# Kernel optimization log

Hardware: AMD Instinct MI355X
Metric: run time of the kernel (lower is better)

The kernel has to match this reference:

```python
import jax, jax.numpy as jnp
import numpy as np

N = 2048      # agent_num
H = 2048      # hid_size
OBS = 1024    # obs_size
A = 64        # action_dim
ITERS = 3     # comm_iters
B = 1         # batch (structurally 1: original does gate.view(1,n,n))
STD = 0.02


def setup_inputs() -> dict:
    key = jax.random.key(0)
    ks = jax.random.split(key, 10)
    f = lambda k, shp: (jax.random.normal(k, shp, jnp.float32) * STD)
    return {
        "obs": jax.random.normal(ks[0], (B, N, OBS), jnp.float32),
        "alive_mask": jnp.ones((N,), jnp.float32),
        "enc_w": f(ks[1], (H, OBS)),
        "enc_b": jnp.zeros((H,), jnp.float32),
        "g_w": f(ks[2], (N, H)),
        "g_b": jnp.zeros((N,), jnp.float32),
        "w_ih": f(ks[3], (4 * H, H)),
        "w_hh": f(ks[4], (4 * H, H)),
        "b_ih": f(ks[5], (4 * H,)),
        "b_hh": f(ks[6], (4 * H,)),
        "act_w": f(ks[7], (A, H)),
        "act_b": jnp.zeros((A,), jnp.float32),
        "val_w": f(ks[8], (1, H)),
        "val_b": jnp.zeros((1,), jnp.float32),
    }


def reference(obs, alive_mask, enc_w, enc_b, g_w, g_b, w_ih, w_hh,
              b_ih, b_hh, act_w, act_b, val_w, val_b):
    b, n, _ = obs.shape
    hid = enc_w.shape[0]
    # state encoder: tanh(Linear(obs))
    e = jnp.tanh(jnp.einsum('bno,ho->bnh', obs, enc_w) + enc_b)  # (B,n,H)
    h = jnp.zeros((b, n, hid), obs.dtype)
    cell = jnp.zeros((b, n, hid), obs.dtype)
    comm_mask = 1.0 - jnp.eye(n, dtype=obs.dtype)                # (n,n), no self-comm
    n_alive = jnp.sum(alive_mask)
    alive_pair = alive_mask[:, None] * alive_mask[None, :]       # alive[j]*alive[i]
    static_w = comm_mask * alive_pair / (n_alive - 1.0)          # (n,n)

    for it in range(ITERS):
        # hard gate: ceil(sigmoid(g(h)))  -> (B, n_sender, n_receiver)
        gate = jnp.ceil(jax.nn.sigmoid(jnp.einsum('bjh,kh->bjk', h, g_w) + g_b))
        G = gate * static_w                                      # (B,n,n)
        # masked gated broadcast-sum over sender agents j (fused, no (B,n,n,H))
        if it == 0:
            c = jnp.zeros_like(h)
        else:
            c = jnp.einsum('bji,bjh->bih', G, h)
        inp = e + c                                              # (B,n,H)
        # torch.nn.LSTMCell, gate order (i, f, g, o)
        z = (jnp.einsum('bnh,gh->bng', inp, w_ih)
             + jnp.einsum('bnh,gh->bng', h, w_hh) + b_ih + b_hh)
        zi, zf, zg, zo = jnp.split(z, 4, axis=-1)
        cell = jax.nn.sigmoid(zf) * cell + jax.nn.sigmoid(zi) * jnp.tanh(zg)
        h = jax.nn.sigmoid(zo) * jnp.tanh(cell)

    log_p = jax.nn.log_softmax(jnp.einsum('bnh,ah->bna', h, act_w) + act_b, axis=-1)
    value = jnp.einsum('bnh,vh->bnv', h, val_w) + val_b
    return log_p, value
```

## Files before the change

### kernel.cpp

```cpp
#include <hip/hip_runtime.h>
#include <cmath>

#define N_AG 2048
#define HID  2048
#define OBSD 1024
#define ACT  64
#define GATES (4*HID)

typedef short s16x8 __attribute__((ext_vector_type(8)));
typedef short s16x4 __attribute__((ext_vector_type(4)));
typedef float f32x4 __attribute__((ext_vector_type(4)));

__device__ __forceinline__ unsigned short f2bf(float f) {
  union { float f; unsigned u; } v; v.f = f;
  return (unsigned short)((v.u + 0x7FFFu + ((v.u >> 16) & 1u)) >> 16);
}
__device__ __forceinline__ float bf2f(unsigned short u) {
  union { float f; unsigned u; } v; v.u = ((unsigned)u) << 16;
  return v.f;
}
__device__ __forceinline__ float sigm(float x) { return 1.0f / (1.0f + expf(-x)); }

__device__ __forceinline__ void gload16(const unsigned short* g, unsigned short* l) {
  __builtin_amdgcn_global_load_lds(
      (const __attribute__((address_space(1))) void*)g,
      (__attribute__((address_space(3))) void*)l, 16, 0, 0);
}


template <int MODE>
__global__ __launch_bounds__(512, 2) void gemm256(
    const unsigned short* __restrict__ A, const unsigned short* __restrict__ B,
    int K, int lda, int ldb,
    unsigned short* __restrict__ E1b, const float* __restrict__ q,
    const float* __restrict__ bc, float* __restrict__ cell,
    unsigned short* __restrict__ hN)
{
  __shared__ __align__(16) unsigned short As[32768];
  __shared__ __align__(16) unsigned short Bs[32768];

  const int tid  = threadIdx.x;
  const int lane = tid & 63;
  const int wave = tid >> 6;
  const int wm   = wave >> 2, wn = wave & 3;
  const int quad = lane >> 4, l16 = lane & 15, r7 = lane & 7;
  const long tileM = (long)blockIdx.y * 256;
  const long tileN = (long)blockIdx.x * 256;

  const unsigned scol  = (((lane & 7) ^ (lane >> 3)) * 8u);
  const unsigned aoffL = (unsigned)(tileM + wave * 8 + (lane >> 3)) * (unsigned)lda + scol;
  const unsigned boffL = (unsigned)(tileN + (wave >> 2) * 64 + (wave & 3) * 8 + (lane >> 3))
                           * (unsigned)ldb + scol;

#define ST_A(d, h, t) { \
    gload16(A + aoffL + (unsigned)((h) * 64) * (unsigned)lda + (unsigned)(t) * 64u, \
            &As[(d) * 16384 + (h) * 8192 + wave * 512]); \
    gload16(A + aoffL + (unsigned)(128 + (h) * 64) * (unsigned)lda + (unsigned)(t) * 64u, \
            &As[(d) * 16384 + (h) * 8192 + wave * 512 + 4096]); }
#define ST_B(d, h, t) { \
    gload16(B + boffL + (unsigned)((h) * 32) * (unsigned)ldb + (unsigned)(t) * 64u, \
            &Bs[(d) * 16384 + (h) * 8192 + wave * 512]); \
    gload16(B + boffL + (unsigned)(128 + (h) * 32) * (unsigned)ldb + (unsigned)(t) * 64u, \
            &Bs[(d) * 16384 + (h) * 8192 + wave * 512 + 4096]); }

  const int ax = wm * 4096 + l16 * 64;
  const int bx = wn * 2048 + l16 * 64;
  const int c0 = (quad ^ r7) * 8;
  const int c1 = ((4 + quad) ^ r7) * 8;

  s16x8 af0[4][2], af1[4][2], bA[2][2], bB[2][2];
  f32x4 acc[8][4] = {};

#define LD_A(d, Mh, dst) { const unsigned short* p_ = &As[(d) * 16384 + (Mh) * 8192 + ax]; \
    _Pragma("unroll") for (int ml = 0; ml < 4; ++ml) { \
      dst[ml][0] = *(const s16x8*)(p_ + ml * 1024 + c0); \
      dst[ml][1] = *(const s16x8*)(p_ + ml * 1024 + c1); } }
#define LD_B(d, Nh, dst) { const unsigned short* p_ = &Bs[(d) * 16384 + (Nh) * 8192 + bx]; \
    _Pragma("unroll") for (int nl = 0; nl < 2; ++nl) { \
      dst[nl][0] = *(const s16x8*)(p_ + nl * 1024 + c0); \
      dst[nl][1] = *(const s16x8*)(p_ + nl * 1024 + c1); } }
#define QMM(Mh, Nh, afv, bb) \
    _Pragma("unroll") for (int ks = 0; ks < 2; ++ks) \
    _Pragma("unroll") for (int ml = 0; ml < 4; ++ml) \
    _Pragma("unroll") for (int nl = 0; nl < 2; ++nl) \
      acc[(Mh) * 4 + ml][(Nh) * 2 + nl] = __builtin_amdgcn_mfma_f32_16x16x32_bf16( \
          afv[ml][ks], bb[nl][ks], acc[(Mh) * 4 + ml][(Nh) * 2 + nl], 0, 0, 0);
#define BAR  __builtin_amdgcn_s_barrier()
#define SCHB __builtin_amdgcn_sched_barrier(0)

  const int NT = K >> 6;

  ST_B(0, 0, 0); ST_A(0, 0, 0); ST_B(0, 1, 0); ST_A(0, 1, 0);
  asm volatile("s_waitcnt vmcnt(0)" ::: "memory");
  BAR;
  LD_A(0, 0, af0); LD_B(0, 0, bA);

  for (int t = 0; t < NT; ++t) {
    const int cur = t & 1, nxt = cur ^ 1;
    const bool s1 = (t + 1 < NT);
    LD_B(cur, 1, bB);
    if (s1) { ST_B(nxt, 0, t + 1); ST_A(nxt, 0, t + 1); }
    SCHB;
    __builtin_amdgcn_s_setprio(1); QMM(0, 0, af0, bA); __builtin_amdgcn_s_setprio(0);
    if (s1) { asm volatile("s_waitcnt vmcnt(4)" ::: "memory"); }
    else    { asm volatile("s_waitcnt vmcnt(0)" ::: "memory"); }
    BAR;
    LD_A(cur, 1, af1);
    if (s1) ST_B(nxt, 1, t + 1);
    SCHB;
    __builtin_amdgcn_s_setprio(1); QMM(0, 1, af0, bB); __builtin_amdgcn_s_setprio(0);
    if (s1) { asm volatile("s_waitcnt vmcnt(2)" ::: "memory"); }
    BAR;
    if (s1) ST_A(nxt, 1, t + 1);
    SCHB;
    __builtin_amdgcn_s_setprio(1); QMM(1, 0, af1, bA); __builtin_amdgcn_s_setprio(0);
    if (s1) LD_B(nxt, 0, bA);
    BAR;
    if (s1) LD_A(nxt, 0, af0);
    SCHB;
    __builtin_amdgcn_s_setprio(1); QMM(1, 1, af1, bB); __builtin_amdgcn_s_setprio(0);
    if (s1) { asm volatile("s_waitcnt vmcnt(2)" ::: "memory"); }
    BAR;
  }

  const int cb0 = (int)tileN + wn * 64;
  const int hid = ((cb0 >> 6) << 4) | l16;
  float bcv[4], qv[4];
#pragma unroll
  for (int g = 0; g < 4; ++g) {
    bcv[g] = bc[cb0 + g * 16 + l16];
    qv[g]  = (MODE == 11) ? q[cb0 + g * 16 + l16] : 0.f;
  }
#pragma unroll
  for (int mf = 0; mf < 8; ++mf) {
    long ag0 = tileM + wm * 128 + mf * 16 + quad * 4;
#pragma unroll
    for (int r = 0; r < 4; ++r) {
      long ag = ag0 + r;
      size_t eb_i = (size_t)ag * GATES + cb0 + l16;
      float zi = acc[mf][0][r], zf = acc[mf][1][r];
      float zg = acc[mf][2][r], zo = acc[mf][3][r];
      if (MODE == 10) {
        E1b[eb_i]      = f2bf(zi);
        E1b[eb_i + 16] = f2bf(zf);
        E1b[eb_i + 32] = f2bf(zg);
        E1b[eb_i + 48] = f2bf(zo);
        zi += bcv[0]; zf += bcv[1]; zg += bcv[2]; zo += bcv[3];
      } else {
        zi += bf2f(E1b[eb_i])      + qv[0] + bcv[0];
        zf += bf2f(E1b[eb_i + 16]) + qv[1] + bcv[1];
        zg += bf2f(E1b[eb_i + 32]) + qv[2] + bcv[2];
        zo += bf2f(E1b[eb_i + 48]) + qv[3] + bcv[3];
      }
      float cold = (MODE == 10) ? 0.f : cell[(size_t)ag * HID + hid];
      float cnew = sigm(zf) * cold + sigm(zi) * tanhf(zg);
      float hv   = sigm(zo) * tanhf(cnew);
      cell[(size_t)ag * HID + hid] = cnew;
      hN[(size_t)ag * HID + hid]   = f2bf(hv);
    }
  }
#undef ST_A
#undef ST_B
#undef LD_A
#undef LD_B
#undef QMM
#undef BAR
#undef SCHB
}

template <int MODE>
__global__ __launch_bounds__(256, 4) void gemm_bt(
    const unsigned short* __restrict__ A, const unsigned short* __restrict__ B,
    int K, int lda, int ldb,
    unsigned short* __restrict__ Cb, float* __restrict__ Cf, int ldc,
    const float* __restrict__ bias)
{
  __shared__ __align__(16) unsigned short As0[2 * 128 * 32];
  __shared__ __align__(16) unsigned short Bs0[2 * 128 * 32];
  const int tid  = threadIdx.x;
  const int lane = tid & 63;
  const int wave = tid >> 6;
  const int wm = wave >> 1, wn = wave & 1;
  const int quad = lane >> 4, l16 = lane & 15;
  const long tileM = (long)blockIdx.y * 128;
  const long tileN = (long)blockIdx.x * 128;
  const long koff  = (long)blockIdx.z * K;

  const int srow = lane >> 2;
  const int skc  = (lane & 3) * 8;
  const unsigned short* gA = &A[(tileM + wave * 32 + srow) * lda + koff + skc];
  const unsigned short* gB = &B[(tileN + wave * 32 + srow) * ldb + koff + skc];
  const int ldsOff = wave * 32 * 32;

  f32x4 acc[4][4] = {};
  const int nIt = K >> 5;

  gload16(gA, &As0[ldsOff]);
  gload16(gA + 16 * lda, &As0[ldsOff + 16 * 32]);
  gload16(gB, &Bs0[ldsOff]);
  gload16(gB + 16 * ldb, &Bs0[ldsOff + 16 * 32]);

  for (int i = 0; i < nIt; ++i) {
    __syncthreads();
    const int cb = (i & 1) * 4096;
    if (i + 1 < nIt) {
      const int nb = ((i + 1) & 1) * 4096;
      const long ko = (long)(i + 1) * 32;
      gload16(gA + ko, &As0[nb + ldsOff]);
      gload16(gA + ko + 16 * lda, &As0[nb + ldsOff + 16 * 32]);
      gload16(gB + ko, &Bs0[nb + ldsOff]);
      gload16(gB + ko + 16 * ldb, &Bs0[nb + ldsOff + 16 * 32]);
    }
    s16x8 af[4], bfr[4];
#pragma unroll
    for (int ii = 0; ii < 4; ++ii)
      af[ii] = *(const s16x8*)&As0[cb + (wm * 64 + ii * 16 + l16) * 32 + quad * 8];
#pragma unroll
    for (int j = 0; j < 4; ++j)
      bfr[j] = *(const s16x8*)&Bs0[cb + (wn * 64 + j * 16 + l16) * 32 + quad * 8];
#pragma unroll
    for (int ii = 0; ii < 4; ++ii)
#pragma unroll
      for (int j = 0; j < 4; ++j)
        acc[ii][j] = __builtin_amdgcn_mfma_f32_16x16x32_bf16(af[ii], bfr[j], acc[ii][j], 0, 0, 0);
  }

#pragma unroll
  for (int i = 0; i < 4; ++i) {
    long r0 = tileM + wm * 64 + i * 16 + quad * 4;
#pragma unroll
    for (int j = 0; j < 4; ++j) {
      long col = tileN + wn * 64 + j * 16 + l16;
      float bv = (MODE == 1) ? bias[col] : 0.f;
#pragma unroll
      for (int r = 0; r < 4; ++r) {
        float v = acc[i][j][r];
        if (MODE == 1) { v = tanhf(v + bv); Cb[(r0 + r) * ldc + col] = f2bf(v); }
        if (MODE == 2) atomicAdd(&Cf[(r0 + r) * ldc + col], v);
      }
    }
  }
}

__global__ void cvt4_dual(const float* __restrict__ inA, unsigned short* __restrict__ outA,
                          const float* __restrict__ inB, unsigned short* __restrict__ outB) {
  int i = blockIdx.x * 256 + threadIdx.x;
  f32x4 a = ((const f32x4*)inA)[i];
  f32x4 b = ((const f32x4*)inB)[i];
  s16x4 oa, ob;
#pragma unroll
  for (int c = 0; c < 4; ++c) { oa[c] = (short)f2bf(a[c]); ob[c] = (short)f2bf(b[c]); }
  ((s16x4*)outA)[i] = oa;
  ((s16x4*)outB)[i] = ob;
}

__global__ void buildw(const float* __restrict__ w_ih, const float* __restrict__ w_hh,
                       const float* __restrict__ nA,
                       unsigned short* __restrict__ Wihb, unsigned short* __restrict__ W2b) {
  int i = blockIdx.x * 256 + threadIdx.x;
  float s = 1.0f / (nA[0] - 1.0f);
  int c  = i >> 9;
  int kk = (i & 511) * 4;
  int g   = (c >> 4) & 3;
  int hid = ((c >> 6) << 4) | (c & 15);
  size_t src = ((size_t)g * HID + hid) * HID + kk;
  size_t dst = (size_t)c * HID + kk;
  f32x4 a = *(const f32x4*)&w_ih[src];
  f32x4 b = *(const f32x4*)&w_hh[src];
  s16x4 oa, ob;
#pragma unroll
  for (int e = 0; e < 4; ++e) {
    oa[e] = (short)f2bf(a[e]);
    ob[e] = (short)f2bf(b[e] - s * a[e]);
  }
  *(s16x4*)&Wihb[dst] = oa;
  *(s16x4*)&W2b[dst] = ob;
}

__global__ void build_whd(const float* __restrict__ act_w, const float* __restrict__ val_w,
                          unsigned short* __restrict__ whd) {
  int i = blockIdx.x * 256 + threadIdx.x;
  int r = i >> 9;
  int k = (i & 511) * 4;
  f32x4 v = {0.f, 0.f, 0.f, 0.f};
  if (r < 64)       v = *(const f32x4*)&act_w[(size_t)r * HID + k];
  else if (r == 64) v = *(const f32x4*)&val_w[k];
  s16x4 o;
  o[0] = (short)f2bf(v[0]); o[1] = (short)f2bf(v[1]);
  o[2] = (short)f2bf(v[2]); o[3] = (short)f2bf(v[3]);
  *(s16x4*)&whd[(size_t)r * HID + k] = o;
}

__global__ void biasmix(const float* __restrict__ b_ih, const float* __restrict__ b_hh,
                        float* __restrict__ bc) {
  int i = blockIdx.x * 256 + threadIdx.x;
  if (i < GATES) {
    int g   = (i >> 4) & 3;
    int hid = ((i >> 6) << 4) | (i & 15);
    int src = g * HID + hid;
    bc[i] = b_ih[src] + b_hh[src];
  }
}

__global__ void nalive_k(const float* __restrict__ alive, float* __restrict__ nA) {
  __shared__ float red[256];
  float s = 0.f;
  for (int i = threadIdx.x; i < N_AG; i += 256) s += alive[i];
  red[threadIdx.x] = s;
  __syncthreads();
  for (int st = 128; st > 0; st >>= 1) {
    if (threadIdx.x < st) red[threadIdx.x] += red[threadIdx.x + st];
    __syncthreads();
  }
  if (threadIdx.x == 0) nA[0] = red[0];
}

__global__ void colsum(const unsigned short* __restrict__ hb, const float* __restrict__ alive,
                       float* __restrict__ S) {
  int hid = blockIdx.x * 256 + threadIdx.x;
  int r0 = blockIdx.y * 128;
  float s = 0.f;
  for (int n = r0; n < r0 + 128; ++n) s += alive[n] * bf2f(hb[(size_t)n * HID + hid]);
  atomicAdd(&S[hid], s);
}

__global__ __launch_bounds__(256) void gemv_q(const unsigned short* __restrict__ Wihb,
                                              const float* __restrict__ S,
                                              const float* __restrict__ nA,
                                              float* __restrict__ q) {
  __shared__ float Sl[HID];
  int tid = threadIdx.x, lane = tid & 63, wave = tid >> 6;
  for (int k = tid; k < HID; k += 256) Sl[k] = S[k];
  __syncthreads();
  int g = blockIdx.x * 4 + wave;
  const unsigned short* wr = Wihb + (size_t)g * HID;
  float acc = 0.f;
#pragma unroll
  for (int c = 0; c < 4; ++c) {
    int k = c * 512 + lane * 8;
    s16x8 w = *(const s16x8*)&wr[k];
#pragma unroll
    for (int e = 0; e < 8; ++e) acc += bf2f((unsigned short)w[e]) * Sl[k + e];
  }
  for (int off = 32; off; off >>= 1) acc += __shfl_xor(acc, off);
  if (lane == 0) q[g] = acc / (nA[0] - 1.0f);
}

__global__ __launch_bounds__(256) void head_ep(const float* __restrict__ zh,
                                               const float* __restrict__ act_b,
                                               const float* __restrict__ val_b,
                                               float* __restrict__ out) {
  int wave = threadIdx.x >> 6, lane = threadIdx.x & 63;
  int row = blockIdx.x * 4 + wave;
  const float* zr = zh + (size_t)row * 128;
  float a = zr[lane] + act_b[lane];
  float m = a;
  for (int off = 32; off; off >>= 1) m = fmaxf(m, __shfl_xor(m, off));
  float ex = expf(a - m), s = ex;
  for (int off = 32; off; off >>= 1) s += __shfl_xor(s, off);
  out[(size_t)row * ACT + lane] = a - m - logf(s);
  if (lane == 0) out[(size_t)N_AG * ACT + row] = zr[64] + val_b[0];
}

extern "C" void kernel_launch(void* const* d_in, const int* in_sizes, int n_in,
                              void* d_out, int out_size, void* d_ws, size_t ws_size,
                              hipStream_t stream) {
  const float* obs   = (const float*)d_in[0];
  const float* alive = (const float*)d_in[1];
  const float* enc_w = (const float*)d_in[2];
  const float* enc_b = (const float*)d_in[3];
  const float* w_ih  = (const float*)d_in[6];
  const float* w_hh  = (const float*)d_in[7];
  const float* b_ih  = (const float*)d_in[8];
  const float* b_hh  = (const float*)d_in[9];
  const float* act_w = (const float*)d_in[10];
  const float* act_b = (const float*)d_in[11];
  const float* val_w = (const float*)d_in[12];
  const float* val_b = (const float*)d_in[13];
  float* out = (float*)d_out;

  char* p = (char*)d_ws;
  unsigned short* Wihb = (unsigned short*)p; p += (size_t)GATES * HID * 2;
  unsigned short* W2b  = (unsigned short*)p; p += (size_t)GATES * HID * 2;
  unsigned short* E1b  = (unsigned short*)p; p += (size_t)N_AG * GATES * 2;
  unsigned short* obsb = (unsigned short*)p; p += (size_t)N_AG * OBSD * 2;
  unsigned short* encb = (unsigned short*)p; p += (size_t)HID * OBSD * 2;
  unsigned short* eb   = (unsigned short*)p; p += (size_t)N_AG * HID * 2;
  unsigned short* h0   = (unsigned short*)p; p += (size_t)N_AG * HID * 2;
  unsigned short* h1   = (unsigned short*)p; p += (size_t)N_AG * HID * 2;
  unsigned short* Whd  = (unsigned short*)p; p += (size_t)128 * HID * 2;
  float* cell = (float*)p; p += (size_t)N_AG * HID * 4;
  float* zh   = (float*)p; p += (size_t)N_AG * 128 * 4;
  float* bc   = (float*)p; p += GATES * 4;
  float* q    = (float*)p; p += GATES * 4;
  float* S    = (float*)p; p += HID * 4;
  float* nA   = (float*)p; p += 256;

  cvt4_dual<<<(N_AG * OBSD / 4) / 256, 256, 0, stream>>>(obs, obsb, enc_w, encb);
  nalive_k<<<1, 256, 0, stream>>>(alive, nA);
  buildw<<<((size_t)GATES * HID / 4) / 256, 256, 0, stream>>>(w_ih, w_hh, nA, Wihb, W2b);
  build_whd<<<(128 * HID / 4) / 256, 256, 0, stream>>>(act_w, val_w, Whd);
  biasmix<<<GATES / 256, 256, 0, stream>>>(b_ih, b_hh, bc);

  gemm_bt<1><<<dim3(HID / 128, N_AG / 128), 256, 0, stream>>>(
      obsb, encb, OBSD, OBSD, OBSD, eb, nullptr, HID, enc_b);

  gemm256<10><<<dim3(GATES / 256, N_AG / 256), 512, 0, stream>>>(
      eb, Wihb, HID, HID, HID, E1b, nullptr, bc, cell, h0);

  unsigned short* hcur = h0;
  unsigned short* hnxt = h1;
  for (int it = 1; it < 3; ++it) {
    hipMemsetAsync(S, 0, HID * 4, stream);
    colsum<<<dim3(HID / 256, 16), 256, 0, stream>>>(hcur, alive, S);
    gemv_q<<<GATES / 4, 256, 0, stream>>>(Wihb, S, nA, q);
    gemm256<11><<<dim3(GATES / 256, N_AG / 256), 512, 0, stream>>>(
        hcur, W2b, HID, HID, HID, E1b, q, bc, cell, hnxt);
    unsigned short* tmp = hcur; hcur = hnxt; hnxt = tmp;
  }

  hipMemsetAsync(zh, 0, (size_t)N_AG * 128 * 4, stream);
  gemm_bt<2><<<dim3(1, N_AG / 128, 8), 256, 0, stream>>>(
      hcur, Whd, HID / 8, HID, HID, nullptr, zh, 128, nullptr);
  head_ep<<<N_AG / 4, 256, 0, stream>>>(zh, act_b, val_b, out);
}
```

Baseline: 537.2 us.

## Fuse alive-weighted column sum into LSTM GEMM epilogue and pack per-thread state

The separate colsum kernel is removed. Each LSTM GEMM epilogue now accumulates alive-weighted h values and atomically adds them into a per-iteration S buffer, which saves a pass over h and two launches. The E1b and cell buffers are re-laid out in a per-block, per-thread packed order so epilogue reads and writes are contiguous vector accesses instead of strided scalar ones. Sigmoid and tanh switch to fast exp/rcp approximations, trading some accuracy, and the sum now uses fp32 h rather than the bf16-rounded value.

Result: faster. 477.6 us (-11.1%).

```diff
diff --git a/kernel.cpp b/kernel.cpp
--- a/kernel.cpp
+++ b/kernel.cpp
@@ -19,7 +19,12 @@
   union { float f; unsigned u; } v; v.u = ((unsigned)u) << 16;
   return v.f;
 }
-__device__ __forceinline__ float sigm(float x) { return 1.0f / (1.0f + expf(-x)); }
+__device__ __forceinline__ float fsigm(float x) {
+  return __builtin_amdgcn_rcpf(1.0f + __expf(-x));
+}
+__device__ __forceinline__ float ftanh(float x) {
+  return 2.0f * __builtin_amdgcn_rcpf(1.0f + __expf(-2.0f * x)) - 1.0f;
+}
 
 __device__ __forceinline__ void gload16(const unsigned short* g, unsigned short* l) {
   __builtin_amdgcn_global_load_lds(
@@ -28,13 +33,14 @@
 }
 
 
-template <int MODE>
+template <int MODE, int ACCS>
 __global__ __launch_bounds__(512, 2) void gemm256(
     const unsigned short* __restrict__ A, const unsigned short* __restrict__ B,
     int K, int lda, int ldb,
     unsigned short* __restrict__ E1b, const float* __restrict__ q,
     const float* __restrict__ bc, float* __restrict__ cell,
-    unsigned short* __restrict__ hN)
+    unsigned short* __restrict__ hN,
+    const float* __restrict__ alive, float* __restrict__ S)
 {
   __shared__ __align__(16) unsigned short As[32768];
   __shared__ __align__(16) unsigned short Bs[32768];
@@ -125,39 +131,48 @@
 
   const int cb0 = (int)tileN + wn * 64;
   const int hid = ((cb0 >> 6) << 4) | l16;
+  const int bid = (int)blockIdx.y * (int)gridDim.x + (int)blockIdx.x;
   float bcv[4], qv[4];
 #pragma unroll
   for (int g = 0; g < 4; ++g) {
     bcv[g] = bc[cb0 + g * 16 + l16];
     qv[g]  = (MODE == 11) ? q[cb0 + g * 16 + l16] : 0.f;
   }
+  float sacc = 0.f;
 #pragma unroll
   for (int mf = 0; mf < 8; ++mf) {
     long ag0 = tileM + wm * 128 + mf * 16 + quad * 4;
 #pragma unroll
     for (int r = 0; r < 4; ++r) {
       long ag = ag0 + r;
-      size_t eb_i = (size_t)ag * GATES + cb0 + l16;
+      const size_t pk = ((size_t)bid * 32 + (mf * 4 + r)) * 512 + tid;
       float zi = acc[mf][0][r], zf = acc[mf][1][r];
       float zg = acc[mf][2][r], zo = acc[mf][3][r];
       if (MODE == 10) {
-        E1b[eb_i]      = f2bf(zi);
-        E1b[eb_i + 16] = f2bf(zf);
-        E1b[eb_i + 32] = f2bf(zg);
-        E1b[eb_i + 48] = f2bf(zo);
+        s16x4 ev;
+        ev[0] = (short)f2bf(zi); ev[1] = (short)f2bf(zf);
+        ev[2] = (short)f2bf(zg); ev[3] = (short)f2bf(zo);
+        *(s16x4*)&E1b[pk * 4] = ev;
         zi += bcv[0]; zf += bcv[1]; zg += bcv[2]; zo += bcv[3];
       } else {
-        zi += bf2f(E1b[eb_i])      + qv[0] + bcv[0];
-        zf += bf2f(E1b[eb_i + 16]) + qv[1] + bcv[1];
-        zg += bf2f(E1b[eb_i + 32]) + qv[2] + bcv[2];
-        zo += bf2f(E1b[eb_i + 48]) + qv[3] + bcv[3];
+        s16x4 ev = *(const s16x4*)&E1b[pk * 4];
+        zi += bf2f((unsigned short)ev[0]) + qv[0] + bcv[0];
+        zf += bf2f((unsigned short)ev[1]) + qv[1] + bcv[1];
+        zg += bf2f((unsigned short)ev[2]) + qv[2] + bcv[2];
+        zo += bf2f((unsigned short)ev[3]) + qv[3] + bcv[3];
       }
-      float cold = (MODE == 10) ? 0.f : cell[(size_t)ag * HID + hid];
-      float cnew = sigm(zf) * cold + sigm(zi) * tanhf(zg);
-      float hv   = sigm(zo) * tanhf(cnew);
-      cell[(size_t)ag * HID + hid] = cnew;
-      hN[(size_t)ag * HID + hid]   = f2bf(hv);
+      float cold = (MODE == 10) ? 0.f : cell[pk];
+      float cnew = fsigm(zf) * cold + fsigm(zi) * ftanh(zg);
+      float hv   = fsigm(zo) * ftanh(cnew);
+      cell[pk] = cnew;
+      hN[(size_t)ag * HID + hid] = f2bf(hv);
+      if (ACCS) sacc += alive[ag] * hv;
     }
+  }
+  if (ACCS) {
+    sacc += __shfl_xor(sacc, 16);
+    sacc += __shfl_xor(sacc, 32);
+    if (quad == 0) atomicAdd(&S[hid], sacc);
   }
 #undef ST_A
 #undef ST_B
@@ -235,7 +250,7 @@
 #pragma unroll
       for (int r = 0; r < 4; ++r) {
         float v = acc[i][j][r];
-        if (MODE == 1) { v = tanhf(v + bv); Cb[(r0 + r) * ldc + col] = f2bf(v); }
+        if (MODE == 1) { v = ftanh(v + bv); Cb[(r0 + r) * ldc + col] = f2bf(v); }
         if (MODE == 2) atomicAdd(&Cf[(r0 + r) * ldc + col], v);
       }
     }
@@ -313,15 +328,6 @@
     __syncthreads();
   }
   if (threadIdx.x == 0) nA[0] = red[0];
-}
-
-__global__ void colsum(const unsigned short* __restrict__ hb, const float* __restrict__ alive,
-                       float* __restrict__ S) {
-  int hid = blockIdx.x * 256 + threadIdx.x;
-  int r0 = blockIdx.y * 128;
-  float s = 0.f;
-  for (int n = r0; n < r0 + 128; ++n) s += alive[n] * bf2f(hb[(size_t)n * HID + hid]);
-  atomicAdd(&S[hid], s);
 }
 
 __global__ __launch_bounds__(256) void gemv_q(const unsigned short* __restrict__ Wihb,
@@ -393,34 +399,33 @@
   float* zh   = (float*)p; p += (size_t)N_AG * 128 * 4;
   float* bc   = (float*)p; p += GATES * 4;
   float* q    = (float*)p; p += GATES * 4;
-  float* S    = (float*)p; p += HID * 4;
+  float* S12  = (float*)p; p += 2 * HID * 4;
   float* nA   = (float*)p; p += 256;
+  float* S1 = S12, *S2 = S12 + HID;
 
   cvt4_dual<<<(N_AG * OBSD / 4) / 256, 256, 0, stream>>>(obs, obsb, enc_w, encb);
   nalive_k<<<1, 256, 0, stream>>>(alive, nA);
   buildw<<<((size_t)GATES * HID / 4) / 256, 256, 0, stream>>>(w_ih, w_hh, nA, Wihb, W2b);
   build_whd<<<(128 * HID / 4) / 256, 256, 0, stream>>>(act_w, val_w, Whd);
   biasmix<<<GATES / 256, 256, 0, stream>>>(b_ih, b_hh, bc);
+  hipMemsetAsync(S12, 0, 2 * HID * 4, stream);
+  hipMemsetAsync(zh, 0, (size_t)N_AG * 128 * 4, stream);
 
   gemm_bt<1><<<dim3(HID / 128, N_AG / 128), 256, 0, stream>>>(
       obsb, encb, OBSD, OBSD, OBSD, eb, nullptr, HID, enc_b);
 
-  gemm256<10><<<dim3(GATES / 256, N_AG / 256), 512, 0, stream>>>(
-      eb, Wihb, HID, HID, HID, E1b, nullptr, bc, cell, h0);
-
-  unsigned short* hcur = h0;
-  unsigned short* hnxt = h1;
-  for (int it = 1; it < 3; ++it) {
-    hipMemsetAsync(S, 0, HID * 4, stream);
-    colsum<<<dim3(HID / 256, 16), 256, 0, stream>>>(hcur, alive, S);
-    gemv_q<<<GATES / 4, 256, 0, stream>>>(Wihb, S, nA, q);
-    gemm256<11><<<dim3(GATES / 256, N_AG / 256), 512, 0, stream>>>(
-        hcur, W2b, HID, HID, HID, E1b, q, bc, cell, hnxt);
-    unsigned short* tmp = hcur; hcur = hnxt; hnxt = tmp;
-  }
-
-  hipMemsetAsync(zh, 0, (size_t)N_AG * 128 * 4, stream);
+  gemm256<10, 1><<<dim3(GATES / 256, N_AG / 256), 512, 0, stream>>>(
+      eb, Wihb, HID, HID, HID, E1b, nullptr, bc, cell, h0, alive, S1);
+
+  gemv_q<<<GATES / 4, 256, 0, stream>>>(Wihb, S1, nA, q);
+  gemm256<11, 1><<<dim3(GATES / 256, N_AG / 256), 512, 0, stream>>>(
+      h0, W2b, HID, HID, HID, E1b, q, bc, cell, h1, alive, S2);
+
+  gemv_q<<<GATES / 4, 256, 0, stream>>>(Wihb, S2, nA, q);
+  gemm256<11, 0><<<dim3(GATES / 256, N_AG / 256), 512, 0, stream>>>(
+      h1, W2b, HID, HID, HID, E1b, q, bc, cell, h0, alive, nullptr);
+
   gemm_bt<2><<<dim3(1, N_AG / 128, 8), 256, 0, stream>>>(
-      hcur, Whd, HID / 8, HID, HID, nullptr, zh, 128, nullptr);
+      h0, Whd, HID / 8, HID, HID, nullptr, zh, 128, nullptr);
   head_ep<<<N_AG / 4, 256, 0, stream>>>(zh, act_b, val_b, out);
 }
```
